# Performance work log

Measured on AMD Instinct MI355X. Metric: run time of the kernel, lower is better.

The kernel has to match this reference:

```python
import jax, jax.numpy as jnp
import numpy as np
from jax import lax

P = 16          # patch size
C = 1024        # embed dim
NH = 8          # heads
HD = C // NH    # head dim = 128


def setup_inputs() -> dict:
    key = jax.random.key(0)
    ks = jax.random.split(key, 12)
    B = 64
    s = 0.02
    return {
        "x": jax.random.normal(ks[0], (B, 1, 256, 256), jnp.float32),
        "conv_w": jax.random.normal(ks[1], (C, 1, P, P), jnp.float32) * s,
        "conv_b": jnp.zeros((C,), jnp.float32),
        "Wq": jax.random.normal(ks[2], (C, C), jnp.float32) * s,
        "bq": jnp.zeros((C,), jnp.float32),
        "Wk": jax.random.normal(ks[3], (C, C), jnp.float32) * s,
        "bk": jnp.zeros((C,), jnp.float32),
        "Wv": jax.random.normal(ks[4], (C, C), jnp.float32) * s,
        "bv": jnp.zeros((C,), jnp.float32),
        "Wp": jax.random.normal(ks[5], (C, C), jnp.float32) * s,
        "bp": jnp.zeros((C,), jnp.float32),
    }


def _forward(x, conv_w, conv_b, Wq, bq, Wk, bk, Wv, bv, Wp, bp):
    # PatchEmbed: 16x16 stride-16 conv -> [B, C, 16, 16]
    h = lax.conv_general_dilated(
        x, conv_w, window_strides=(P, P), padding="VALID",
        dimension_numbers=("NCHW", "OIHW", "NCHW"))
    h = h + conv_b[None, :, None, None]
    B = h.shape[0]
    T = h.shape[2] * h.shape[3]  # 256
    tok = h.reshape(B, C, T).transpose(0, 2, 1)  # [B, T, C]

    def heads(W, b):
        y = jnp.einsum("btc,cd->btd", tok, W) + b
        return y.reshape(B, T, NH, HD).transpose(0, 2, 1, 3)  # [B, H, T, D]

    q, k, v = heads(Wq, bq), heads(Wk, bk), heads(Wv, bv)
    present = jnp.stack((k, v))  # [2, B, H, T, D]

    att = jnp.einsum("bhqd,bhkd->bhqk", q, k) * (1.0 / np.sqrt(HD))
    causal = jnp.tril(jnp.ones((T, T), bool))
    att = jnp.where(causal[None, None], att, -jnp.inf)
    att = jax.nn.softmax(att, axis=-1)  # dropout: eval mode (identity)

    y = jnp.einsum("bhqk,bhkd->bhqd", att, v)
    y = y.transpose(0, 2, 1, 3).reshape(B, T, C)
    y = jnp.einsum("btc,cd->btd", y, Wp) + bp  # resid dropout: identity
    return y, present


def reference(x, conv_w, conv_b, Wq, bq, Wk, bk, Wv, bv, Wp, bp):
    return _forward(x, conv_w, conv_b, Wq, bq, Wk, bk, Wv, bv, Wp, bp)
```

## Files before the change

kernel.cpp:

```cpp
#include <hip/hip_runtime.h>


typedef unsigned short u16;
typedef unsigned int u32;
typedef __attribute__((ext_vector_type(8))) short bf16x8;
typedef __attribute__((ext_vector_type(4))) float f32x4;
typedef __attribute__((ext_vector_type(4))) u16 u16x4;

#define Y_ELEMS  16777216
#define KV_ELEMS 16777216

__device__ __forceinline__ u16 f2b(float f) {
  u32 u = __float_as_uint(f);
  u32 r = u + 0x7fffu + ((u >> 16) & 1u);
  return (u16)(r >> 16);
}

__device__ __forceinline__ float b2f(u16 h) {
  return __uint_as_float(((u32)h) << 16);
}

__device__ __forceinline__ void gl_lds16(const u16* g, u16* l) {
  __builtin_amdgcn_global_load_lds(
      (__attribute__((address_space(1))) void*)g,
      (__attribute__((address_space(3))) void*)l, 16, 0, 0);
}

__global__ __launch_bounds__(256) void patchify_kernel(
    const float* __restrict__ x, u16* __restrict__ ap) {
  int tid = blockIdx.x * 256 + threadIdx.x;
  float4 v = ((const float4*)x)[tid];
  int col4 = tid & 63;
  int row  = (tid >> 6) & 255;
  int b    = tid >> 14;
  int py = row >> 4, ky = row & 15;
  int col = col4 << 2;
  int px = col >> 4, kx = col & 15;
  size_t dst = ((size_t)(b * 256 + py * 16 + px)) * 256 + ky * 16 + kx;
  u16x4 o = { f2b(v.x), f2b(v.y), f2b(v.z), f2b(v.w) };
  *(u16x4*)(ap + dst) = o;
}

__global__ __launch_bounds__(256) void transpose_wc_kernel(
    const float* __restrict__ W, u16* __restrict__ o) {
  __shared__ float tile[32][33];
  int x0 = blockIdx.x * 32, y0 = blockIdx.y * 32;
  int tx = threadIdx.x, ty = threadIdx.y;
#pragma unroll
  for (int i = ty; i < 32; i += 8)
    tile[i][tx] = W[(size_t)(y0 + i) * 256 + x0 + tx];
  __syncthreads();
#pragma unroll
  for (int i = ty; i < 32; i += 8)
    o[(size_t)(x0 + i) * 1024 + y0 + tx] = f2b(tile[tx][i]);
}

__global__ __launch_bounds__(256) void transpose_w_kernel(
    const float* __restrict__ Wq, const float* __restrict__ Wk,
    const float* __restrict__ Wv, const float* __restrict__ Wp,
    u16* __restrict__ Wqkv_t, u16* __restrict__ Wp_t) {
  __shared__ float tile[32][33];
  int z = blockIdx.z;
  const float* W = (z == 0) ? Wq : (z == 1) ? Wk : (z == 2) ? Wv : Wp;
  u16* dst = (z < 3) ? (Wqkv_t + (size_t)z * 1024 * 1024) : Wp_t;
  int x0 = blockIdx.x * 32, y0 = blockIdx.y * 32;
  int tx = threadIdx.x, ty = threadIdx.y;
#pragma unroll
  for (int i = ty; i < 32; i += 8)
    tile[i][tx] = W[(size_t)(y0 + i) * 1024 + x0 + tx];
  __syncthreads();
#pragma unroll
  for (int i = ty; i < 32; i += 8)
    dst[(size_t)(x0 + i) * 1024 + y0 + tx] = f2b(tile[tx][i]);
}

__global__ __launch_bounds__(256) void bias_fold_kernel(
    const u16* __restrict__ Wqkv_t, const float* __restrict__ conv_b,
    const float* __restrict__ bq, const float* __restrict__ bk,
    const float* __restrict__ bv, float* __restrict__ bias_f) {
  int lane = threadIdx.x & 63, w = threadIdx.x >> 6;
  int n = blockIdx.x * 4 + w;
  const u16* row = Wqkv_t + (size_t)n * 1024 + lane * 16;
  const float* cb = conv_b + lane * 16;
  bf16x8 a0 = *(const bf16x8*)row;
  bf16x8 a1 = *(const bf16x8*)(row + 8);
  float s = 0.f;
#pragma unroll
  for (int e = 0; e < 8; ++e) s += b2f((u16)a0[e]) * cb[e];
#pragma unroll
  for (int e = 0; e < 8; ++e) s += b2f((u16)a1[e]) * cb[8 + e];
#pragma unroll
  for (int off = 1; off < 64; off <<= 1) s += __shfl_xor(s, off, 64);
  if (lane == 0) {
    int seg = n >> 10, j = n & 1023;
    float base = (seg == 0 ? bq : seg == 1 ? bk : bv)[j];
    bias_f[n] = base + s;
  }
}

__global__ __launch_bounds__(256) void gemm_kernel(
    const u16* __restrict__ A, const u16* __restrict__ Bt,
    int K, int N, int mode, const float* __restrict__ bias0,
    u16* __restrict__ ob0, u16* __restrict__ ob1, u16* __restrict__ ob2,
    float* __restrict__ of0) {
  __shared__ __attribute__((aligned(16))) char smem[17408];
  u16* As = (u16*)smem;
  u16* Bs = (u16*)(smem + 8192);
  const int t = threadIdx.x;
  const int rr = t >> 2;
  const int c8 = (t & 3) << 3;
  const int lane = t & 63;
  const int w = t >> 6;
  const int wm = (w & 1) << 6, wn = (w >> 1) << 6;
  const int l15 = lane & 15, quad = lane >> 4;
  const int tile_m = blockIdx.x * 128, tile_n = blockIdx.y * 128;

  f32x4 acc[4][4];
  f32x4 zero = {0.f, 0.f, 0.f, 0.f};
#pragma unroll
  for (int i = 0; i < 4; ++i)
#pragma unroll
    for (int j = 0; j < 4; ++j) acc[i][j] = zero;

  const u16* gA0 = A + (size_t)(tile_m + rr) * K + c8;
  const u16* gA1 = A + (size_t)(tile_m + 64 + rr) * K + c8;
  const u16* gB0 = Bt + (size_t)(tile_n + rr) * K + c8;
  const u16* gB1 = Bt + (size_t)(tile_n + 64 + rr) * K + c8;
  u16* lA0 = As + rr * 32 + c8;
  u16* lA1 = As + (64 + rr) * 32 + c8;
  u16* lB0 = Bs + rr * 32 + c8;
  u16* lB1 = Bs + (64 + rr) * 32 + c8;

  for (int k0 = 0; k0 < K; k0 += 32) {
    __syncthreads();
    gl_lds16(gA0 + k0, lA0);
    gl_lds16(gA1 + k0, lA1);
    gl_lds16(gB0 + k0, lB0);
    gl_lds16(gB1 + k0, lB1);
    __syncthreads();
    bf16x8 af[4], bfr[4];
#pragma unroll
    for (int i = 0; i < 4; ++i)
      af[i] = *(const bf16x8*)(As + (wm + 16 * i + l15) * 32 + quad * 8);
#pragma unroll
    for (int j = 0; j < 4; ++j)
      bfr[j] = *(const bf16x8*)(Bs + (wn + 16 * j + l15) * 32 + quad * 8);
#pragma unroll
    for (int i = 0; i < 4; ++i)
#pragma unroll
      for (int j = 0; j < 4; ++j)
        acc[i][j] = __builtin_amdgcn_mfma_f32_16x16x32_bf16(af[i], bfr[j], acc[i][j], 0, 0, 0);
  }

  __syncthreads();
  float* ep = (float*)smem + w * 1088;
  const int ncol = wn + quad * 16;

  f32x4 ba[4];
  if (bias0) {
#pragma unroll
    for (int c = 0; c < 4; ++c)
      ba[c] = *(const f32x4*)(bias0 + tile_n + ncol + c * 4);
  } else {
#pragma unroll
    for (int c = 0; c < 4; ++c) ba[c] = zero;
  }

  int seg = 0, h = 0, dd = 0;
  u16* ob = ob0;
  float* pf = of0;
  if (mode == 1) {
    seg = tile_n >> 10;
    ob = (seg == 0) ? ob0 : (seg == 1) ? ob1 : ob2;
    pf = of0 + (size_t)(seg ? (seg - 1) : 0) * KV_ELEMS;
    int nloc = (tile_n & 1023) + ncol;
    h = nloc >> 7;
    dd = nloc & 127;
  }

#pragma unroll
  for (int i = 0; i < 4; ++i) {
#pragma unroll
    for (int j = 0; j < 4; ++j)
#pragma unroll
      for (int r = 0; r < 4; ++r)
        ep[(quad * 4 + r) * 68 + j * 16 + l15] = acc[i][j][r];
    asm volatile("s_waitcnt lgkmcnt(0)" ::: "memory");
    f32x4 vt[4];
#pragma unroll
    for (int c = 0; c < 4; ++c) {
      vt[c] = *(const f32x4*)(ep + l15 * 68 + quad * 16 + c * 4);
      vt[c] += ba[c];
    }
    asm volatile("s_waitcnt lgkmcnt(0)" ::: "memory");
    const int m = tile_m + wm + 16 * i + l15;

    bf16x8 h0, h1;
#pragma unroll
    for (int e = 0; e < 8; ++e) h0[e] = (short)f2b(vt[e >> 2][e & 3]);
#pragma unroll
    for (int e = 0; e < 8; ++e) h1[e] = (short)f2b(vt[2 + (e >> 2)][e & 3]);

    if (mode == 1) {
      int bb = m >> 8, tt = m & 255;
      size_t idx = ((size_t)(bb * 8 + h) * 256 + tt) * 128 + dd;
      *(bf16x8*)(ob + idx) = h0;
      *(bf16x8*)(ob + idx + 8) = h1;
      if (seg) {
#pragma unroll
        for (int c = 0; c < 4; ++c) *(f32x4*)(pf + idx + c * 4) = vt[c];
      }
    } else if (mode == 2) {
      float* p = of0 + (size_t)m * N + tile_n + ncol;
#pragma unroll
      for (int c = 0; c < 4; ++c) *(f32x4*)(p + c * 4) = vt[c];
    } else {
      u16* p = ob0 + (size_t)m * N + tile_n + ncol;
      *(bf16x8*)p = h0;
      *(bf16x8*)(p + 8) = h1;
    }
  }
}

__global__ __launch_bounds__(256) void attn_kernel(
    const u16* __restrict__ qw, const u16* __restrict__ kw,
    const u16* __restrict__ vw, u16* __restrict__ yatt) {
  __shared__ __attribute__((aligned(16))) u16 Ks[64 * 136];
  __shared__ __attribute__((aligned(16))) u16 Vs[128 * 72];
  __shared__ __attribute__((aligned(16))) u16 Ps[4 * 16 * 72];
  const int qb = blockIdx.x;
  const int bh = blockIdx.y;
  const int t = threadIdx.x;
  const int lane = t & 63, w = t >> 6;
  const int l15 = lane & 15, quad = lane >> 4;
  const int qrow0 = qb * 64 + w * 16;

  bf16x8 aq[4];
#pragma unroll
  for (int ks = 0; ks < 4; ++ks)
    aq[ks] = *(const bf16x8*)(qw + ((size_t)bh * 256 + qrow0 + l15) * 128 + ks * 32 + quad * 8);

  f32x4 o[8];
  f32x4 zero = {0.f, 0.f, 0.f, 0.f};
#pragma unroll
  for (int dt = 0; dt < 8; ++dt) o[dt] = zero;
  float mi[4] = {-1e30f, -1e30f, -1e30f, -1e30f};
  float li[4] = {0.f, 0.f, 0.f, 0.f};

  const int jp = (t & 31) * 2;
  const int db = (t >> 5) * 16;

  for (int j = 0; j <= qb; ++j) {
    __syncthreads();
    {
      const u16* ksrc = kw + ((size_t)bh * 256 + j * 64) * 128;
      int kr = t >> 2, kc = t & 3;
#pragma unroll
      for (int s = 0; s < 4; ++s) {
        int cb = s * 4 + kc;
        *(bf16x8*)(Ks + kr * 136 + cb * 8) = *(const bf16x8*)(ksrc + kr * 128 + cb * 8);
      }
      const u16* vsrc = vw + ((size_t)bh * 256 + j * 64) * 128;
      bf16x8 r0a = *(const bf16x8*)(vsrc + (size_t)jp * 128 + db);
      bf16x8 r0b = *(const bf16x8*)(vsrc + (size_t)jp * 128 + db + 8);
      bf16x8 r1a = *(const bf16x8*)(vsrc + (size_t)(jp + 1) * 128 + db);
      bf16x8 r1b = *(const bf16x8*)(vsrc + (size_t)(jp + 1) * 128 + db + 8);
#pragma unroll
      for (int dv = 0; dv < 8; ++dv) {
        u32 p = (u32)(u16)r0a[dv] | ((u32)(u16)r1a[dv] << 16);
        *(u32*)(Vs + (db + dv) * 72 + jp) = p;
      }
#pragma unroll
      for (int dv = 0; dv < 8; ++dv) {
        u32 p = (u32)(u16)r0b[dv] | ((u32)(u16)r1b[dv] << 16);
        *(u32*)(Vs + (db + 8 + dv) * 72 + jp) = p;
      }
    }
    __syncthreads();

    f32x4 s4[4];
#pragma unroll
    for (int nt = 0; nt < 4; ++nt) s4[nt] = zero;
#pragma unroll
    for (int nt = 0; nt < 4; ++nt)
#pragma unroll
      for (int ks = 0; ks < 4; ++ks) {
        bf16x8 bk8 = *(const bf16x8*)(Ks + (nt * 16 + l15) * 136 + ks * 32 + quad * 8);
        s4[nt] = __builtin_amdgcn_mfma_f32_16x16x32_bf16(aq[ks], bk8, s4[nt], 0, 0, 0);
      }

    const float sc = 0.08838834764831845f;
    const bool diag = (j == qb);
#pragma unroll
    for (int nt = 0; nt < 4; ++nt) {
      int coln = j * 64 + nt * 16 + l15;
#pragma unroll
      for (int r = 0; r < 4; ++r) {
        float sv = s4[nt][r] * sc;
        if (diag && coln > (qrow0 + quad * 4 + r)) sv = -1e30f;
        s4[nt][r] = sv;
      }
    }

#pragma unroll
    for (int r = 0; r < 4; ++r) {
      float mx = fmaxf(fmaxf(s4[0][r], s4[1][r]), fmaxf(s4[2][r], s4[3][r]));
#pragma unroll
      for (int off = 1; off < 16; off <<= 1)
        mx = fmaxf(mx, __shfl_xor(mx, off, 64));
      float mnew = fmaxf(mi[r], mx);
      float alpha = __expf(mi[r] - mnew);
      float sum = 0.f;
#pragma unroll
      for (int nt = 0; nt < 4; ++nt) {
        float p = __expf(s4[nt][r] - mnew);
        s4[nt][r] = p;
        sum += p;
      }
#pragma unroll
      for (int off = 1; off < 16; off <<= 1)
        sum += __shfl_xor(sum, off, 64);
      li[r] = li[r] * alpha + sum;
      mi[r] = mnew;
#pragma unroll
      for (int dt = 0; dt < 8; ++dt) o[dt][r] *= alpha;
    }

    u16* pw = Ps + w * 16 * 72;
#pragma unroll
    for (int nt = 0; nt < 4; ++nt)
#pragma unroll
      for (int r = 0; r < 4; ++r)
        pw[(quad * 4 + r) * 72 + nt * 16 + l15] = f2b(s4[nt][r]);
    asm volatile("s_waitcnt lgkmcnt(0)" ::: "memory");

    bf16x8 ap[2];
#pragma unroll
    for (int k2 = 0; k2 < 2; ++k2)
      ap[k2] = *(const bf16x8*)(pw + l15 * 72 + k2 * 32 + quad * 8);
#pragma unroll
    for (int dt = 0; dt < 8; ++dt)
#pragma unroll
      for (int k2 = 0; k2 < 2; ++k2) {
        bf16x8 bv8 = *(const bf16x8*)(Vs + (dt * 16 + l15) * 72 + k2 * 32 + quad * 8);
        o[dt] = __builtin_amdgcn_mfma_f32_16x16x32_bf16(ap[k2], bv8, o[dt], 0, 0, 0);
      }
  }

  const int b = bh >> 3, h = bh & 7;
#pragma unroll
  for (int r = 0; r < 4; ++r) {
    float inv = 1.0f / li[r];
    int tt = qrow0 + quad * 4 + r;
    size_t rowbase = ((size_t)b * 256 + tt) * 1024 + h * 128;
#pragma unroll
    for (int dt = 0; dt < 8; ++dt)
      yatt[rowbase + dt * 16 + l15] = f2b(o[dt][r] * inv);
  }
}

extern "C" void kernel_launch(void* const* d_in, const int* in_sizes, int n_in,
                              void* d_out, int out_size, void* d_ws, size_t ws_size,
                              hipStream_t stream) {
  const float* x      = (const float*)d_in[0];
  const float* conv_w = (const float*)d_in[1];
  const float* conv_b = (const float*)d_in[2];
  const float* Wq     = (const float*)d_in[3];
  const float* bq     = (const float*)d_in[4];
  const float* Wk     = (const float*)d_in[5];
  const float* bk     = (const float*)d_in[6];
  const float* Wv     = (const float*)d_in[7];
  const float* bv     = (const float*)d_in[8];
  const float* Wp     = (const float*)d_in[9];
  const float* bp     = (const float*)d_in[10];
  float* out = (float*)d_out;

  char* ws = (char*)d_ws;
  u16*   A_patch = (u16*)(ws);
  u16*   Wc_t    = (u16*)(ws + (8u << 20));
  u16*   W2      = (u16*)(ws + (8u << 20) + (1u << 19));
  float* bias_f  = (float*)(ws + (10u << 20));
  u16*   Wqkv_t  = (u16*)(ws + (10u << 20) + (1u << 16));
  u16*   y_att   = (u16*)(ws);
  u16*   Wp_t    = (u16*)(ws + (32u << 20));
  u16*   q_ws    = (u16*)(ws + (34u << 20));
  u16*   k_ws    = (u16*)(ws + (66u << 20));
  u16*   v_ws    = (u16*)(ws + (98u << 20));

  patchify_kernel<<<4096, 256, 0, stream>>>(x, A_patch);
  transpose_wc_kernel<<<dim3(8, 32), dim3(32, 8), 0, stream>>>(conv_w, Wc_t);
  transpose_w_kernel<<<dim3(32, 32, 4), dim3(32, 8), 0, stream>>>(
      Wq, Wk, Wv, Wp, Wqkv_t, Wp_t);
  bias_fold_kernel<<<768, 256, 0, stream>>>(Wqkv_t, conv_b, bq, bk, bv, bias_f);
  gemm_kernel<<<dim3(24, 2), 256, 0, stream>>>(
      Wqkv_t, Wc_t, 1024, 256, 0, nullptr,
      W2, nullptr, nullptr, nullptr);
  gemm_kernel<<<dim3(128, 24), 256, 0, stream>>>(
      A_patch, W2, 256, 3072, 1, bias_f,
      q_ws, k_ws, v_ws, out + Y_ELEMS);
  attn_kernel<<<dim3(4, 512), 256, 0, stream>>>(q_ws, k_ws, v_ws, y_att);
  gemm_kernel<<<dim3(128, 8), 256, 0, stream>>>(
      y_att, Wp_t, 1024, 1024, 2, bp,
      nullptr, nullptr, nullptr, out);
}
```

Baseline: 464.4 us.

## Double-buffer GEMM LDS, drop bf16 K/V copies, and remap attention blocks

```diff
diff --git a/kernel.cpp b/kernel.cpp
--- a/kernel.cpp
+++ b/kernel.cpp
@@ -41,33 +41,24 @@
   *(u16x4*)(ap + dst) = o;
 }
 
-__global__ __launch_bounds__(256) void transpose_wc_kernel(
-    const float* __restrict__ W, u16* __restrict__ o) {
-  __shared__ float tile[32][33];
-  int x0 = blockIdx.x * 32, y0 = blockIdx.y * 32;
-  int tx = threadIdx.x, ty = threadIdx.y;
-#pragma unroll
-  for (int i = ty; i < 32; i += 8)
-    tile[i][tx] = W[(size_t)(y0 + i) * 256 + x0 + tx];
-  __syncthreads();
-#pragma unroll
-  for (int i = ty; i < 32; i += 8)
-    o[(size_t)(x0 + i) * 1024 + y0 + tx] = f2b(tile[tx][i]);
-}
-
 __global__ __launch_bounds__(256) void transpose_w_kernel(
     const float* __restrict__ Wq, const float* __restrict__ Wk,
     const float* __restrict__ Wv, const float* __restrict__ Wp,
-    u16* __restrict__ Wqkv_t, u16* __restrict__ Wp_t) {
+    const float* __restrict__ Wc, u16* __restrict__ Wqkv_t,
+    u16* __restrict__ Wp_t, u16* __restrict__ Wc_t) {
   __shared__ float tile[32][33];
   int z = blockIdx.z;
-  const float* W = (z == 0) ? Wq : (z == 1) ? Wk : (z == 2) ? Wv : Wp;
-  u16* dst = (z < 3) ? (Wqkv_t + (size_t)z * 1024 * 1024) : Wp_t;
   int x0 = blockIdx.x * 32, y0 = blockIdx.y * 32;
+  if (z == 4 && x0 >= 256) return;
+  const float* W = (z == 0) ? Wq : (z == 1) ? Wk : (z == 2) ? Wv
+                 : (z == 3) ? Wp : Wc;
+  u16* dst = (z < 3) ? (Wqkv_t + (size_t)z * 1024 * 1024)
+           : (z == 3) ? Wp_t : Wc_t;
+  const int stride = (z == 4) ? 256 : 1024;
   int tx = threadIdx.x, ty = threadIdx.y;
 #pragma unroll
   for (int i = ty; i < 32; i += 8)
-    tile[i][tx] = W[(size_t)(y0 + i) * 1024 + x0 + tx];
+    tile[i][tx] = W[(size_t)(y0 + i) * stride + x0 + tx];
   __syncthreads();
 #pragma unroll
   for (int i = ty; i < 32; i += 8)
@@ -101,11 +92,12 @@
 __global__ __launch_bounds__(256) void gemm_kernel(
     const u16* __restrict__ A, const u16* __restrict__ Bt,
     int K, int N, int mode, const float* __restrict__ bias0,
-    u16* __restrict__ ob0, u16* __restrict__ ob1, u16* __restrict__ ob2,
-    float* __restrict__ of0) {
-  __shared__ __attribute__((aligned(16))) char smem[17408];
-  u16* As = (u16*)smem;
-  u16* Bs = (u16*)(smem + 8192);
+    u16* __restrict__ ob0, float* __restrict__ of0) {
+  __shared__ __attribute__((aligned(16))) char smem[32768];
+  u16* As0 = (u16*)smem;
+  u16* Bs0 = (u16*)(smem + 8192);
+  u16* As1 = (u16*)(smem + 16384);
+  u16* Bs1 = (u16*)(smem + 24576);
   const int t = threadIdx.x;
   const int rr = t >> 2;
   const int c8 = (t & 3) << 3;
@@ -126,33 +118,44 @@
   const u16* gA1 = A + (size_t)(tile_m + 64 + rr) * K + c8;
   const u16* gB0 = Bt + (size_t)(tile_n + rr) * K + c8;
   const u16* gB1 = Bt + (size_t)(tile_n + 64 + rr) * K + c8;
-  u16* lA0 = As + rr * 32 + c8;
-  u16* lA1 = As + (64 + rr) * 32 + c8;
-  u16* lB0 = Bs + rr * 32 + c8;
-  u16* lB1 = Bs + (64 + rr) * 32 + c8;
-
-  for (int k0 = 0; k0 < K; k0 += 32) {
-    __syncthreads();
-    gl_lds16(gA0 + k0, lA0);
-    gl_lds16(gA1 + k0, lA1);
-    gl_lds16(gB0 + k0, lB0);
-    gl_lds16(gB1 + k0, lB1);
-    __syncthreads();
+  const int lo0 = rr * 32 + c8;
+  const int lo1 = (64 + rr) * 32 + c8;
+
+  gl_lds16(gA0, As0 + lo0);
+  gl_lds16(gA1, As0 + lo1);
+  gl_lds16(gB0, Bs0 + lo0);
+  gl_lds16(gB1, Bs0 + lo1);
+  __syncthreads();
+
+  int cur = 0;
+  for (int k0 = 0; k0 < K; k0 += 32, cur ^= 1) {
+    u16* Asc = cur ? As1 : As0;
+    u16* Bsc = cur ? Bs1 : Bs0;
+    if (k0 + 32 < K) {
+      u16* Asn = cur ? As0 : As1;
+      u16* Bsn = cur ? Bs0 : Bs1;
+      gl_lds16(gA0 + k0 + 32, Asn + lo0);
+      gl_lds16(gA1 + k0 + 32, Asn + lo1);
+      gl_lds16(gB0 + k0 + 32, Bsn + lo0);
+      gl_lds16(gB1 + k0 + 32, Bsn + lo1);
+    }
     bf16x8 af[4], bfr[4];
 #pragma unroll
     for (int i = 0; i < 4; ++i)
-      af[i] = *(const bf16x8*)(As + (wm + 16 * i + l15) * 32 + quad * 8);
+      af[i] = *(const bf16x8*)(Asc + (wm + 16 * i + l15) * 32 + quad * 8);
 #pragma unroll
     for (int j = 0; j < 4; ++j)
-      bfr[j] = *(const bf16x8*)(Bs + (wn + 16 * j + l15) * 32 + quad * 8);
+      bfr[j] = *(const bf16x8*)(Bsc + (wn + 16 * j + l15) * 32 + quad * 8);
+    __builtin_amdgcn_s_setprio(1);
 #pragma unroll
     for (int i = 0; i < 4; ++i)
 #pragma unroll
       for (int j = 0; j < 4; ++j)
         acc[i][j] = __builtin_amdgcn_mfma_f32_16x16x32_bf16(af[i], bfr[j], acc[i][j], 0, 0, 0);
-  }
-
-  __syncthreads();
+    __builtin_amdgcn_s_setprio(0);
+    __syncthreads();
+  }
+
   float* ep = (float*)smem + w * 1088;
   const int ncol = wn + quad * 16;
 
@@ -167,16 +170,15 @@
   }
 
   int seg = 0, h = 0, dd = 0;
-  u16* ob = ob0;
   float* pf = of0;
   if (mode == 1) {
     seg = tile_n >> 10;
-    ob = (seg == 0) ? ob0 : (seg == 1) ? ob1 : ob2;
     pf = of0 + (size_t)(seg ? (seg - 1) : 0) * KV_ELEMS;
     int nloc = (tile_n & 1023) + ncol;
     h = nloc >> 7;
     dd = nloc & 127;
   }
+  const bool need_bf = (mode == 0) || (mode == 1 && seg == 0);
 
 #pragma unroll
   for (int i = 0; i < 4; ++i) {
@@ -196,17 +198,20 @@
     const int m = tile_m + wm + 16 * i + l15;
 
     bf16x8 h0, h1;
-#pragma unroll
-    for (int e = 0; e < 8; ++e) h0[e] = (short)f2b(vt[e >> 2][e & 3]);
-#pragma unroll
-    for (int e = 0; e < 8; ++e) h1[e] = (short)f2b(vt[2 + (e >> 2)][e & 3]);
+    if (need_bf) {
+#pragma unroll
+      for (int e = 0; e < 8; ++e) h0[e] = (short)f2b(vt[e >> 2][e & 3]);
+#pragma unroll
+      for (int e = 0; e < 8; ++e) h1[e] = (short)f2b(vt[2 + (e >> 2)][e & 3]);
+    }
 
     if (mode == 1) {
       int bb = m >> 8, tt = m & 255;
       size_t idx = ((size_t)(bb * 8 + h) * 256 + tt) * 128 + dd;
-      *(bf16x8*)(ob + idx) = h0;
-      *(bf16x8*)(ob + idx + 8) = h1;
-      if (seg) {
+      if (seg == 0) {
+        *(bf16x8*)(ob0 + idx) = h0;
+        *(bf16x8*)(ob0 + idx + 8) = h1;
+      } else {
 #pragma unroll
         for (int c = 0; c < 4; ++c) *(f32x4*)(pf + idx + c * 4) = vt[c];
       }
@@ -223,13 +228,16 @@
 }
 
 __global__ __launch_bounds__(256) void attn_kernel(
-    const u16* __restrict__ qw, const u16* __restrict__ kw,
-    const u16* __restrict__ vw, u16* __restrict__ yatt) {
+    const u16* __restrict__ qw, const float* __restrict__ kf,
+    const float* __restrict__ vf, u16* __restrict__ yatt) {
   __shared__ __attribute__((aligned(16))) u16 Ks[64 * 136];
   __shared__ __attribute__((aligned(16))) u16 Vs[128 * 72];
   __shared__ __attribute__((aligned(16))) u16 Ps[4 * 16 * 72];
-  const int qb = blockIdx.x;
-  const int bh = blockIdx.y;
+  const int id = blockIdx.x;
+  const int xr = id & 7;
+  const int kk = id >> 3;
+  const int qb = kk & 3;
+  const int bh = ((kk >> 2) << 3) + xr;
   const int t = threadIdx.x;
   const int lane = t & 63, w = t >> 6;
   const int l15 = lane & 15, quad = lane >> 4;
@@ -249,38 +257,47 @@
 
   const int jp = (t & 31) * 2;
   const int db = (t >> 5) * 16;
+  const int kr = t >> 2, kc = t & 3;
+  const float* kbase = kf + (size_t)bh * 256 * 128;
+  const float* vbase = vf + (size_t)bh * 256 * 128;
 
   for (int j = 0; j <= qb; ++j) {
     __syncthreads();
     {
-      const u16* ksrc = kw + ((size_t)bh * 256 + j * 64) * 128;
-      int kr = t >> 2, kc = t & 3;
+      const float* ksrc = kbase + (size_t)j * 64 * 128;
 #pragma unroll
       for (int s = 0; s < 4; ++s) {
-        int cb = s * 4 + kc;
-        *(bf16x8*)(Ks + kr * 136 + cb * 8) = *(const bf16x8*)(ksrc + kr * 128 + cb * 8);
-      }
-      const u16* vsrc = vw + ((size_t)bh * 256 + j * 64) * 128;
-      bf16x8 r0a = *(const bf16x8*)(vsrc + (size_t)jp * 128 + db);
-      bf16x8 r0b = *(const bf16x8*)(vsrc + (size_t)jp * 128 + db + 8);
-      bf16x8 r1a = *(const bf16x8*)(vsrc + (size_t)(jp + 1) * 128 + db);
-      bf16x8 r1b = *(const bf16x8*)(vsrc + (size_t)(jp + 1) * 128 + db + 8);
-#pragma unroll
-      for (int dv = 0; dv < 8; ++dv) {
-        u32 p = (u32)(u16)r0a[dv] | ((u32)(u16)r1a[dv] << 16);
-        *(u32*)(Vs + (db + dv) * 72 + jp) = p;
-      }
-#pragma unroll
-      for (int dv = 0; dv < 8; ++dv) {
-        u32 p = (u32)(u16)r0b[dv] | ((u32)(u16)r1b[dv] << 16);
-        *(u32*)(Vs + (db + 8 + dv) * 72 + jp) = p;
-      }
+        const float* p = ksrc + (size_t)kr * 128 + (s * 4 + kc) * 8;
+        f32x4 a = *(const f32x4*)p;
+        f32x4 b = *(const f32x4*)(p + 4);
+        bf16x8 wv;
+#pragma unroll
+        for (int e = 0; e < 4; ++e) wv[e] = (short)f2b(a[e]);
+#pragma unroll
+        for (int e = 0; e < 4; ++e) wv[4 + e] = (short)f2b(b[e]);
+        *(bf16x8*)(Ks + kr * 136 + (s * 4 + kc) * 8) = wv;
+      }
+      const float* vsrc = vbase + (size_t)j * 64 * 128;
+      f32x4 v0[4], v1[4];
+#pragma unroll
+      for (int c = 0; c < 4; ++c) {
+        v0[c] = *(const f32x4*)(vsrc + (size_t)jp * 128 + db + c * 4);
+        v1[c] = *(const f32x4*)(vsrc + (size_t)(jp + 1) * 128 + db + c * 4);
+      }
+#pragma unroll
+      for (int c = 0; c < 4; ++c)
+#pragma unroll
+        for (int e = 0; e < 4; ++e) {
+          u32 p = (u32)f2b(v0[c][e]) | ((u32)f2b(v1[c][e]) << 16);
+          *(u32*)(Vs + (db + c * 4 + e) * 72 + jp) = p;
+        }
     }
     __syncthreads();
 
     f32x4 s4[4];
 #pragma unroll
     for (int nt = 0; nt < 4; ++nt) s4[nt] = zero;
+    __builtin_amdgcn_s_setprio(1);
 #pragma unroll
     for (int nt = 0; nt < 4; ++nt)
 #pragma unroll
@@ -288,6 +305,7 @@
         bf16x8 bk8 = *(const bf16x8*)(Ks + (nt * 16 + l15) * 136 + ks * 32 + quad * 8);
         s4[nt] = __builtin_amdgcn_mfma_f32_16x16x32_bf16(aq[ks], bk8, s4[nt], 0, 0, 0);
       }
+    __builtin_amdgcn_s_setprio(0);
 
     const float sc = 0.08838834764831845f;
     const bool diag = (j == qb);
@@ -338,6 +356,7 @@
 #pragma unroll
     for (int k2 = 0; k2 < 2; ++k2)
       ap[k2] = *(const bf16x8*)(pw + l15 * 72 + k2 * 32 + quad * 8);
+    __builtin_amdgcn_s_setprio(1);
 #pragma unroll
     for (int dt = 0; dt < 8; ++dt)
 #pragma unroll
@@ -345,6 +364,7 @@
         bf16x8 bv8 = *(const bf16x8*)(Vs + (dt * 16 + l15) * 72 + k2 * 32 + quad * 8);
         o[dt] = __builtin_amdgcn_mfma_f32_16x16x32_bf16(ap[k2], bv8, o[dt], 0, 0, 0);
       }
+    __builtin_amdgcn_s_setprio(0);
   }
 
   const int b = bh >> 3, h = bh & 7;
@@ -384,22 +404,19 @@
   u16*   y_att   = (u16*)(ws);
   u16*   Wp_t    = (u16*)(ws + (32u << 20));
   u16*   q_ws    = (u16*)(ws + (34u << 20));
-  u16*   k_ws    = (u16*)(ws + (66u << 20));
-  u16*   v_ws    = (u16*)(ws + (98u << 20));
+
+  float* present_k = out + Y_ELEMS;
+  float* present_v = out + Y_ELEMS + KV_ELEMS;
 
   patchify_kernel<<<4096, 256, 0, stream>>>(x, A_patch);
-  transpose_wc_kernel<<<dim3(8, 32), dim3(32, 8), 0, stream>>>(conv_w, Wc_t);
-  transpose_w_kernel<<<dim3(32, 32, 4), dim3(32, 8), 0, stream>>>(
-      Wq, Wk, Wv, Wp, Wqkv_t, Wp_t);
+  transpose_w_kernel<<<dim3(32, 32, 5), dim3(32, 8), 0, stream>>>(
+      Wq, Wk, Wv, Wp, conv_w, Wqkv_t, Wp_t, Wc_t);
   bias_fold_kernel<<<768, 256, 0, stream>>>(Wqkv_t, conv_b, bq, bk, bv, bias_f);
   gemm_kernel<<<dim3(24, 2), 256, 0, stream>>>(
-      Wqkv_t, Wc_t, 1024, 256, 0, nullptr,
-      W2, nullptr, nullptr, nullptr);
+      Wqkv_t, Wc_t, 1024, 256, 0, nullptr, W2, nullptr);
   gemm_kernel<<<dim3(128, 24), 256, 0, stream>>>(
-      A_patch, W2, 256, 3072, 1, bias_f,
-      q_ws, k_ws, v_ws, out + Y_ELEMS);
-  attn_kernel<<<dim3(4, 512), 256, 0, stream>>>(q_ws, k_ws, v_ws, y_att);
+      A_patch, W2, 256, 3072, 1, bias_f, q_ws, out + Y_ELEMS);
+  attn_kernel<<<2048, 256, 0, stream>>>(q_ws, present_k, present_v, y_att);
   gemm_kernel<<<dim3(128, 8), 256, 0, stream>>>(
-      y_att, Wp_t, 1024, 1024, 2, bp,
-      nullptr, nullptr, nullptr, out);
-}
+      y_att, Wp_t, 1024, 1024, 2, bp, nullptr, out);
+}
```

Result: faster. 430.1 us (-7.4%).
